# Kernel optimization log

Hardware: AMD Instinct MI355X
Metric: run time of the kernel (lower is better)

## Reference

```python
import jax, jax.numpy as jnp
import numpy as np

NUM_USER = 200000
NUM_ITEM = 400000
D = 64
NNZ = 6000000
GCN_LAYER = 3


def setup_inputs() -> dict:
    key = jax.random.key(0)
    k1, k2, k3, k4 = jax.random.split(key, 4)
    n_nodes = NUM_USER + NUM_ITEM
    adj_indices = jax.random.randint(k1, (2, NNZ), 0, n_nodes, dtype=jnp.int32)
    # normalized adjacency values are positive; mimic D^-1/2 A D^-1/2 scale
    adj_values = jax.random.uniform(k2, (NNZ,), dtype=jnp.float32) * 0.1
    user_emb = jax.random.normal(k3, (NUM_USER, D), dtype=jnp.float32) * 0.01
    item_emb = jax.random.normal(k4, (NUM_ITEM, D), dtype=jnp.float32) * 0.01
    return {
        "adj_values": adj_values,
        "user_emb": user_emb,
        "item_emb": item_emb,
        "adj_indices": adj_indices,
        "gcn_layer": GCN_LAYER,
    }


def reference(adj_values, user_emb, item_emb, adj_indices, gcn_layer):
    """LightGCN propagation: gcn_layer hops of SpMM, stack, mean, split."""
    num_user = user_emb.shape[0]
    n_nodes = num_user + item_emb.shape[0]
    row, col = adj_indices[0], adj_indices[1]

    ego = jnp.concatenate([user_emb, item_emb], axis=0)  # [N, D]
    layers = [ego]
    cur = ego
    for _ in range(gcn_layer):  # small fixed layer loop
        # SpMM: out[row] += vals * cur[col]
        msg = adj_values[:, None] * cur[col]  # [nnz, D]
        cur = jax.ops.segment_sum(msg, row, num_segments=n_nodes)  # [N, D]
        layers.append(cur)
    mean_emb = jnp.mean(jnp.stack(layers, axis=1), axis=1)  # [N, D]
    return mean_emb[:num_user], mean_emb[num_user:]
```

## Files before the change

kernel.cpp:

```cpp
#include <hip/hip_runtime.h>
#include <stdint.h>

#define NUM_USER 200000
#define NUM_ITEM 400000
#define NNODES   (NUM_USER + NUM_ITEM)
#define D        64
#define NNZ      6000000
#define ND       ((size_t)NNODES * D)

#define RPB       512
#define NBUCK     ((NNODES + RPB - 1) / RPB)
#define CAP       8192
#define CHUNK     16384

typedef float    f4 __attribute__((ext_vector_type(4)));
typedef uint32_t u4 __attribute__((ext_vector_type(4)));

__device__ __forceinline__ uint32_t bfr(float f) {
    uint32_t u = __float_as_uint(f);
    return (u + 0x7FFFu + ((u >> 16) & 1u)) >> 16;
}
__device__ __forceinline__ uint32_t pack2(float lo, float hi) {
    return (bfr(hi) << 16) | bfr(lo);
}
__device__ __forceinline__ float bl(uint32_t u) { return __uint_as_float(u << 16); }
__device__ __forceinline__ float bh(uint32_t u) { return __uint_as_float(u & 0xFFFF0000u); }

__global__ void k_cvt(const float* __restrict__ uemb, const float* __restrict__ iemb,
                      u4* __restrict__ ego_bf) {
    long long tid = (long long)blockIdx.x * blockDim.x + threadIdx.x;
    if (tid >= (long long)(ND / 8)) return;
    int node = (int)(tid >> 3);
    int seg = (int)(tid & 7);
    const f4* src = (node < NUM_USER)
        ? (const f4*)uemb + ((size_t)node << 4) + seg * 2
        : (const f4*)iemb + ((size_t)(node - NUM_USER) << 4) + seg * 2;
    f4 a = src[0], b = src[1];
    u4 o;
    o.x = pack2(a.x, a.y); o.y = pack2(a.z, a.w);
    o.z = pack2(b.x, b.y); o.w = pack2(b.z, b.w);
    ego_bf[tid] = o;
}


__global__ void k_coarse_hist(const int* __restrict__ rows, int* __restrict__ bcnt) {
    __shared__ int h[NBUCK];
    for (int i = threadIdx.x; i < NBUCK; i += blockDim.x) h[i] = 0;
    __syncthreads();
    int stride = gridDim.x * blockDim.x;
    for (int e = blockIdx.x * blockDim.x + threadIdx.x; e < NNZ; e += stride)
        atomicAdd(&h[rows[e] >> 9], 1);
    __syncthreads();
    for (int i = threadIdx.x; i < NBUCK; i += blockDim.x)
        if (h[i]) atomicAdd(&bcnt[i], h[i]);
}

__global__ void k_bucket_scan(const int* __restrict__ bcnt, int* __restrict__ bbase,
                              int* __restrict__ bcur, int* __restrict__ row_ptr) {
    __shared__ int tsum[1024];
    int t = threadIdx.x;
    int i0 = 2 * t, i1 = 2 * t + 1;
    int c0 = (i0 < NBUCK) ? bcnt[i0] : 0;
    int c1 = (i1 < NBUCK) ? bcnt[i1] : 0;
    tsum[t] = c0 + c1;
    __syncthreads();
    for (int off = 1; off < 1024; off <<= 1) {
        int v = (t >= off) ? tsum[t - off] : 0;
        __syncthreads();
        tsum[t] += v;
        __syncthreads();
    }
    int excl = (t == 0) ? 0 : tsum[t - 1];
    if (i0 < NBUCK) { bbase[i0] = excl;      bcur[i0] = excl; }
    if (i1 < NBUCK) { bbase[i1] = excl + c0; bcur[i1] = excl + c0; }
    if (t == 0) { bbase[NBUCK] = NNZ; row_ptr[NNODES] = NNZ; }
}

__global__ void k_coarse_scatter(const int* __restrict__ rows, const int* __restrict__ cols,
                                 const float* __restrict__ vals, int* __restrict__ bcur,
                                 uint64_t* __restrict__ edges) {
    __shared__ int cnt[NBUCK];
    __shared__ int start[NBUCK];
    int t = threadIdx.x;
    long long base = (long long)blockIdx.x * CHUNK;
    for (int i = t; i < NBUCK; i += blockDim.x) cnt[i] = 0;
    __syncthreads();
    for (int i = t; i < CHUNK; i += blockDim.x) {
        long long e = base + i;
        if (e < NNZ) atomicAdd(&cnt[rows[e] >> 9], 1);
    }
    __syncthreads();
    for (int b = t; b < NBUCK; b += blockDim.x) {
        int c = cnt[b];
        start[b] = c ? atomicAdd(&bcur[b], c) : 0;
    }
    __syncthreads();
    for (int i = t; i < NBUCK; i += blockDim.x) cnt[i] = 0;
    __syncthreads();
    for (int i = t; i < CHUNK; i += blockDim.x) {
        long long e = base + i;
        if (e >= NNZ) continue;
        int r = rows[e];
        int b = r >> 9;
        int pos = start[b] + atomicAdd(&cnt[b], 1);
        uint64_t packed = ((uint64_t)(uint32_t)__float_as_int(vals[e]) << 32)
                        | ((uint64_t)(r & (RPB - 1)) << 20)
                        | (uint32_t)cols[e];
        edges[pos] = packed;
    }
}

__global__ void k_bucket_sort(const int* __restrict__ bbase, uint64_t* __restrict__ edges,
                              int* __restrict__ row_ptr) {
    __shared__ uint64_t stage[CAP];
    __shared__ int hist[RPB];
    __shared__ int cur[RPB];
    int b = blockIdx.x;
    int t = threadIdx.x;
    int bb = bbase[b];
    int cnt = bbase[b + 1] - bb;
    for (int i = t; i < cnt; i += blockDim.x) stage[i] = edges[bb + i];
    for (int i = t; i < RPB; i += blockDim.x) hist[i] = 0;
    __syncthreads();
    for (int i = t; i < cnt; i += blockDim.x)
        atomicAdd(&hist[(uint32_t)(stage[i] >> 20) & (RPB - 1)], 1);
    __syncthreads();
    for (int off = 1; off < RPB; off <<= 1) {
        int v = (t >= off) ? hist[t - off] : 0;
        __syncthreads();
        hist[t] += v;
        __syncthreads();
    }
    int excl = (t == 0) ? 0 : hist[t - 1];
    long long row = (long long)b * RPB + t;
    if (row < NNODES) row_ptr[row] = bb + excl;
    cur[t] = excl;
    __syncthreads();
    for (int i = t; i < cnt; i += blockDim.x) {
        uint64_t e = stage[i];
        int lr = (uint32_t)(e >> 20) & (RPB - 1);
        int pos = atomicAdd(&cur[lr], 1);
        edges[bb + pos] = (e & 0xFFFFFFFF00000000ull) | (e & 0xFFFFFull);
    }
}


template<int EPI, bool FINAL>
__global__ void k_hop(const int* __restrict__ row_ptr,
                      const uint64_t* __restrict__ edges,
                      const u4* __restrict__ src_bf,
                      const u4* __restrict__ ego_bf,
                      const float* __restrict__ uemb,
                      const float* __restrict__ iemb,
                      void* __restrict__ dst) {
    constexpr int U = 8;
    int wave = (blockIdx.x * blockDim.x + threadIdx.x) >> 6;
    int lane = threadIdx.x & 63;
    int g = lane >> 3;
    int l = lane & 7;
    int r = wave * 8 + g;
    bool rv = (r < NNODES);
    int beg = rv ? row_ptr[r] : 0;
    int end = rv ? row_ptr[r + 1] : 0;
    float acc0[8], acc1[8];
    #pragma unroll
    for (int k = 0; k < 8; ++k) { acc0[k] = 0.f; acc1[k] = 0.f; }
    for (int j = beg; ; j += U) {
        if (!__any(j < end)) break;
        uint64_t cv[U];
        bool act[U];
        #pragma unroll
        for (int u = 0; u < U; ++u) {
            act[u] = (j + u < end);
            if (act[u]) cv[u] = edges[j + u];
        }
        u4 s[U];
        #pragma unroll
        for (int u = 0; u < U; ++u) {
            if (act[u]) s[u] = src_bf[((size_t)((uint32_t)cv[u] & 0xFFFFFu) << 3) + l];
        }
        #pragma unroll
        for (int u = 0; u < U; ++u) {
            if (act[u]) {
                float v = __int_as_float((int)(cv[u] >> 32));
                float* a = (u & 1) ? acc1 : acc0;
                a[0] += v * bl(s[u].x); a[1] += v * bh(s[u].x);
                a[2] += v * bl(s[u].y); a[3] += v * bh(s[u].y);
                a[4] += v * bl(s[u].z); a[5] += v * bh(s[u].z);
                a[6] += v * bl(s[u].w); a[7] += v * bh(s[u].w);
            }
        }
    }
    if (!rv) return;
    float e[8];
    if (EPI == 1) {
        u4 eg = ego_bf[((size_t)r << 3) + l];
        e[0] = bl(eg.x); e[1] = bh(eg.x); e[2] = bl(eg.y); e[3] = bh(eg.y);
        e[4] = bl(eg.z); e[5] = bh(eg.z); e[6] = bl(eg.w); e[7] = bh(eg.w);
    } else {
        const f4* ep = (r < NUM_USER)
            ? (const f4*)uemb + ((size_t)r << 4) + l * 2
            : (const f4*)iemb + ((size_t)(r - NUM_USER) << 4) + l * 2;
        f4 e0 = ep[0], e1 = ep[1];
        e[0] = e0.x; e[1] = e0.y; e[2] = e0.z; e[3] = e0.w;
        e[4] = e1.x; e[5] = e1.y; e[6] = e1.z; e[7] = e1.w;
    }
    float res[8];
    #pragma unroll
    for (int k = 0; k < 8; ++k) res[k] = acc0[k] + acc1[k] + e[k];
    if (FINAL) {
        f4 o0 = {res[0] * 0.25f, res[1] * 0.25f, res[2] * 0.25f, res[3] * 0.25f};
        f4 o1 = {res[4] * 0.25f, res[5] * 0.25f, res[6] * 0.25f, res[7] * 0.25f};
        f4* dp = (f4*)dst + ((size_t)r << 4) + l * 2;
        __builtin_nontemporal_store(o0, dp);
        __builtin_nontemporal_store(o1, dp + 1);
    } else {
        u4 o;
        o.x = pack2(res[0], res[1]); o.y = pack2(res[2], res[3]);
        o.z = pack2(res[4], res[5]); o.w = pack2(res[6], res[7]);
        *((u4*)dst + ((size_t)r << 3) + l) = o;
    }
}

extern "C" void kernel_launch(void* const* d_in, const int* in_sizes, int n_in,
                              void* d_out, int out_size, void* d_ws, size_t ws_size,
                              hipStream_t stream) {
    const float* vals = (const float*)d_in[0];
    const float* uemb = (const float*)d_in[1];
    const float* iemb = (const float*)d_in[2];
    const int*   rows = (const int*)d_in[3];
    const int*   cols = rows + NNZ;

    float* out = (float*)d_out;

    size_t off = 0;
    char* ws = (char*)d_ws;
    auto take = [&](size_t bytes) { char* p = ws + off; off += (bytes + 255) & ~(size_t)255; return p; };
    u4*       ego_bf  = (u4*)take((ND / 8) * sizeof(u4));
    u4*       X1      = (u4*)take((ND / 8) * sizeof(u4));
    int*      row_ptr = (int*)take((NNODES + 1) * sizeof(int));
    int*      bcnt    = (int*)take(NBUCK * sizeof(int));
    int*      bbase   = (int*)take((NBUCK + 1) * sizeof(int));
    int*      bcur    = (int*)take(NBUCK * sizeof(int));
    uint64_t* edges   = (uint64_t*)take((size_t)NNZ * sizeof(uint64_t));
    u4*       X2      = (u4*)take((ND / 8) * sizeof(u4));
    bool three_buf = (off <= ws_size);

    const long long cvt_threads = ND / 8;
    k_cvt<<<(int)((cvt_threads + 255) / 256), 256, 0, stream>>>(uemb, iemb, ego_bf);

    hipMemsetAsync(bcnt, 0, NBUCK * sizeof(int), stream);
    k_coarse_hist<<<512, 512, 0, stream>>>(rows, bcnt);
    k_bucket_scan<<<1, 1024, 0, stream>>>(bcnt, bbase, bcur, row_ptr);
    k_coarse_scatter<<<(NNZ + CHUNK - 1) / CHUNK, 512, 0, stream>>>(rows, cols, vals, bcur, edges);
    k_bucket_sort<<<NBUCK, RPB, 0, stream>>>(bbase, edges, row_ptr);

    const int hop_blocks = (NNODES + 31) / 32;
    if (three_buf) {
        k_hop<1, false><<<hop_blocks, 256, 0, stream>>>(row_ptr, edges, ego_bf, ego_bf, uemb, iemb, X1);
        k_hop<1, false><<<hop_blocks, 256, 0, stream>>>(row_ptr, edges, X1,     ego_bf, uemb, iemb, X2);
        k_hop<1, true ><<<hop_blocks, 256, 0, stream>>>(row_ptr, edges, X2,     ego_bf, uemb, iemb, out);
    } else {
        k_hop<1, false><<<hop_blocks, 256, 0, stream>>>(row_ptr, edges, ego_bf, ego_bf, uemb, iemb, X1);
        k_hop<0, false><<<hop_blocks, 256, 0, stream>>>(row_ptr, edges, X1,     nullptr, uemb, iemb, ego_bf);
        k_hop<0, true ><<<hop_blocks, 256, 0, stream>>>(row_ptr, edges, ego_bf, nullptr, uemb, iemb, out);
    }
}
```

Measured before the change: 723.6 us.

## Split feature dimension into two halves so each hop pass gathers a smaller working set

```diff
diff --git a/kernel.cpp b/kernel.cpp
--- a/kernel.cpp
+++ b/kernel.cpp
@@ -27,7 +27,7 @@
 __device__ __forceinline__ float bh(uint32_t u) { return __uint_as_float(u & 0xFFFF0000u); }
 
 __global__ void k_cvt(const float* __restrict__ uemb, const float* __restrict__ iemb,
-                      u4* __restrict__ ego_bf) {
+                      u4* __restrict__ half0, u4* __restrict__ half1) {
     long long tid = (long long)blockIdx.x * blockDim.x + threadIdx.x;
     if (tid >= (long long)(ND / 8)) return;
     int node = (int)(tid >> 3);
@@ -39,7 +39,8 @@
     u4 o;
     o.x = pack2(a.x, a.y); o.y = pack2(a.z, a.w);
     o.z = pack2(b.x, b.y); o.w = pack2(b.z, b.w);
-    ego_bf[tid] = o;
+    u4* dst = (seg < 4) ? half0 : half1;
+    dst[(size_t)node * 4 + (seg & 3)] = o;
 }
 
 
@@ -148,17 +149,18 @@
 template<int EPI, bool FINAL>
 __global__ void k_hop(const int* __restrict__ row_ptr,
                       const uint64_t* __restrict__ edges,
-                      const u4* __restrict__ src_bf,
-                      const u4* __restrict__ ego_bf,
+                      const u4* __restrict__ src_h,
+                      const u4* __restrict__ ego_h,
                       const float* __restrict__ uemb,
                       const float* __restrict__ iemb,
-                      void* __restrict__ dst) {
+                      void* __restrict__ dst,
+                      int h) {
     constexpr int U = 8;
     int wave = (blockIdx.x * blockDim.x + threadIdx.x) >> 6;
     int lane = threadIdx.x & 63;
-    int g = lane >> 3;
-    int l = lane & 7;
-    int r = wave * 8 + g;
+    int g = lane >> 2;
+    int l = lane & 3;
+    int r = wave * 16 + g;
     bool rv = (r < NNODES);
     int beg = rv ? row_ptr[r] : 0;
     int end = rv ? row_ptr[r + 1] : 0;
@@ -177,7 +179,7 @@
         u4 s[U];
         #pragma unroll
         for (int u = 0; u < U; ++u) {
-            if (act[u]) s[u] = src_bf[((size_t)((uint32_t)cv[u] & 0xFFFFFu) << 3) + l];
+            if (act[u]) s[u] = src_h[(size_t)((uint32_t)cv[u] & 0xFFFFFu) * 4 + l];
         }
         #pragma unroll
         for (int u = 0; u < U; ++u) {
@@ -194,13 +196,13 @@
     if (!rv) return;
     float e[8];
     if (EPI == 1) {
-        u4 eg = ego_bf[((size_t)r << 3) + l];
+        u4 eg = ego_h[(size_t)r * 4 + l];
         e[0] = bl(eg.x); e[1] = bh(eg.x); e[2] = bl(eg.y); e[3] = bh(eg.y);
         e[4] = bl(eg.z); e[5] = bh(eg.z); e[6] = bl(eg.w); e[7] = bh(eg.w);
     } else {
-        const f4* ep = (r < NUM_USER)
-            ? (const f4*)uemb + ((size_t)r << 4) + l * 2
-            : (const f4*)iemb + ((size_t)(r - NUM_USER) << 4) + l * 2;
+        const f4* ep = ((r < NUM_USER)
+            ? (const f4*)uemb + ((size_t)r << 4)
+            : (const f4*)iemb + ((size_t)(r - NUM_USER) << 4)) + h * 8 + l * 2;
         f4 e0 = ep[0], e1 = ep[1];
         e[0] = e0.x; e[1] = e0.y; e[2] = e0.z; e[3] = e0.w;
         e[4] = e1.x; e[5] = e1.y; e[6] = e1.z; e[7] = e1.w;
@@ -211,14 +213,14 @@
     if (FINAL) {
         f4 o0 = {res[0] * 0.25f, res[1] * 0.25f, res[2] * 0.25f, res[3] * 0.25f};
         f4 o1 = {res[4] * 0.25f, res[5] * 0.25f, res[6] * 0.25f, res[7] * 0.25f};
-        f4* dp = (f4*)dst + ((size_t)r << 4) + l * 2;
+        f4* dp = (f4*)dst + ((size_t)r << 4) + h * 8 + l * 2;
         __builtin_nontemporal_store(o0, dp);
         __builtin_nontemporal_store(o1, dp + 1);
     } else {
         u4 o;
         o.x = pack2(res[0], res[1]); o.y = pack2(res[2], res[3]);
         o.z = pack2(res[4], res[5]); o.w = pack2(res[6], res[7]);
-        *((u4*)dst + ((size_t)r << 3) + l) = o;
+        *((u4*)dst + (size_t)r * 4 + l) = o;
     }
 }
 
@@ -233,21 +235,26 @@
 
     float* out = (float*)d_out;
 
+    const size_t HALF_U4 = ND / 16;
     size_t off = 0;
     char* ws = (char*)d_ws;
     auto take = [&](size_t bytes) { char* p = ws + off; off += (bytes + 255) & ~(size_t)255; return p; };
-    u4*       ego_bf  = (u4*)take((ND / 8) * sizeof(u4));
-    u4*       X1      = (u4*)take((ND / 8) * sizeof(u4));
+    u4*       egoT    = (u4*)take(2 * HALF_U4 * sizeof(u4));
+    u4*       X1      = (u4*)take(2 * HALF_U4 * sizeof(u4));
     int*      row_ptr = (int*)take((NNODES + 1) * sizeof(int));
     int*      bcnt    = (int*)take(NBUCK * sizeof(int));
     int*      bbase   = (int*)take((NBUCK + 1) * sizeof(int));
     int*      bcur    = (int*)take(NBUCK * sizeof(int));
     uint64_t* edges   = (uint64_t*)take((size_t)NNZ * sizeof(uint64_t));
-    u4*       X2      = (u4*)take((ND / 8) * sizeof(u4));
+    u4*       X2      = (u4*)take(2 * HALF_U4 * sizeof(u4));
     bool three_buf = (off <= ws_size);
 
+    u4* ego_h[2] = { egoT, egoT + HALF_U4 };
+    u4* x1_h[2]  = { X1,   X1   + HALF_U4 };
+    u4* x2_h[2]  = { X2,   X2   + HALF_U4 };
+
     const long long cvt_threads = ND / 8;
-    k_cvt<<<(int)((cvt_threads + 255) / 256), 256, 0, stream>>>(uemb, iemb, ego_bf);
+    k_cvt<<<(int)((cvt_threads + 255) / 256), 256, 0, stream>>>(uemb, iemb, ego_h[0], ego_h[1]);
 
     hipMemsetAsync(bcnt, 0, NBUCK * sizeof(int), stream);
     k_coarse_hist<<<512, 512, 0, stream>>>(rows, bcnt);
@@ -255,14 +262,20 @@
     k_coarse_scatter<<<(NNZ + CHUNK - 1) / CHUNK, 512, 0, stream>>>(rows, cols, vals, bcur, edges);
     k_bucket_sort<<<NBUCK, RPB, 0, stream>>>(bbase, edges, row_ptr);
 
-    const int hop_blocks = (NNODES + 31) / 32;
+    const int hop_blocks = (NNODES + 63) / 64;
     if (three_buf) {
-        k_hop<1, false><<<hop_blocks, 256, 0, stream>>>(row_ptr, edges, ego_bf, ego_bf, uemb, iemb, X1);
-        k_hop<1, false><<<hop_blocks, 256, 0, stream>>>(row_ptr, edges, X1,     ego_bf, uemb, iemb, X2);
-        k_hop<1, true ><<<hop_blocks, 256, 0, stream>>>(row_ptr, edges, X2,     ego_bf, uemb, iemb, out);
+        for (int h = 0; h < 2; ++h)
+            k_hop<1, false><<<hop_blocks, 256, 0, stream>>>(row_ptr, edges, ego_h[h], ego_h[h], uemb, iemb, x1_h[h], h);
+        for (int h = 0; h < 2; ++h)
+            k_hop<1, false><<<hop_blocks, 256, 0, stream>>>(row_ptr, edges, x1_h[h], ego_h[h], uemb, iemb, x2_h[h], h);
+        for (int h = 0; h < 2; ++h)
+            k_hop<1, true ><<<hop_blocks, 256, 0, stream>>>(row_ptr, edges, x2_h[h], ego_h[h], uemb, iemb, out, h);
     } else {
-        k_hop<1, false><<<hop_blocks, 256, 0, stream>>>(row_ptr, edges, ego_bf, ego_bf, uemb, iemb, X1);
-        k_hop<0, false><<<hop_blocks, 256, 0, stream>>>(row_ptr, edges, X1,     nullptr, uemb, iemb, ego_bf);
-        k_hop<0, true ><<<hop_blocks, 256, 0, stream>>>(row_ptr, edges, ego_bf, nullptr, uemb, iemb, out);
-    }
-}
+        for (int h = 0; h < 2; ++h)
+            k_hop<1, false><<<hop_blocks, 256, 0, stream>>>(row_ptr, edges, ego_h[h], ego_h[h], uemb, iemb, x1_h[h], h);
+        for (int h = 0; h < 2; ++h)
+            k_hop<0, false><<<hop_blocks, 256, 0, stream>>>(row_ptr, edges, x1_h[h], nullptr, uemb, iemb, ego_h[h], h);
+        for (int h = 0; h < 2; ++h)
+            k_hop<0, true ><<<hop_blocks, 256, 0, stream>>>(row_ptr, edges, ego_h[h], nullptr, uemb, iemb, out, h);
+    }
+}
```

After: 1.000 ms. 38.2% more time.
